# Kernel tuning notes

Hardware: AMD Instinct MI355X
Metric: run time of the kernel (lower is better)

Reference implementation:

```python
import jax, jax.numpy as jnp
import numpy as np

N = 50000
E = 800000
P = 800000
DIN = 128
HID = 32
HEADS = 4
DOUT = 128
NEG_SLOPE = 0.2


def _gat_conv(x, src, dst, W, a_src, a_dst, bias, heads, C, n):
    # x: [n, in], W: [in, heads*C], a_src/a_dst: [heads, C], bias: [heads*C]
    xw = (x @ W).reshape(n, heads, C)
    alpha_s = (xw * a_src).sum(-1)  # [n, heads]
    alpha_d = (xw * a_dst).sum(-1)  # [n, heads]
    logits = jax.nn.leaky_relu(alpha_s[src] + alpha_d[dst], NEG_SLOPE)  # [e, heads]
    amax = jax.ops.segment_max(logits, dst, num_segments=n)
    ex = jnp.exp(logits - amax[dst])
    denom = jax.ops.segment_sum(ex, dst, num_segments=n)
    alpha = ex / denom[dst]  # segment softmax over incoming edges
    out = jax.ops.segment_sum(xw[src] * alpha[:, :, None], dst, num_segments=n)
    return out.reshape(n, heads * C) + bias


def setup_inputs() -> dict:
    key = jax.random.key(0)
    ks = jax.random.split(key, 16)
    s = 0.05
    inp = {
        "x": jax.random.normal(ks[0], (N, DIN), dtype=jnp.float32),
        "edge_index": jax.random.randint(ks[1], (2, E), 0, N, dtype=jnp.int32),
        "edge_pairs": jax.random.randint(ks[2], (2, P), 0, N, dtype=jnp.int32),
        "W1": jax.random.normal(ks[3], (DIN, HEADS * HID), dtype=jnp.float32) * s,
        "a_src1": jax.random.normal(ks[4], (HEADS, HID), dtype=jnp.float32) * s,
        "a_dst1": jax.random.normal(ks[5], (HEADS, HID), dtype=jnp.float32) * s,
        "b1": jnp.zeros((HEADS * HID,), dtype=jnp.float32),
        "W2": jax.random.normal(ks[6], (HEADS * HID, DOUT), dtype=jnp.float32) * s,
        "a_src2": jax.random.normal(ks[7], (1, DOUT), dtype=jnp.float32) * s,
        "a_dst2": jax.random.normal(ks[8], (1, DOUT), dtype=jnp.float32) * s,
        "b2": jnp.zeros((DOUT,), dtype=jnp.float32),
        "mw1": jax.random.normal(ks[9], (2 * DOUT, DOUT), dtype=jnp.float32) * s,
        "mb1": jnp.zeros((DOUT,), dtype=jnp.float32),
        "mw2": jax.random.normal(ks[10], (DOUT, DOUT // 2), dtype=jnp.float32) * s,
        "mb2": jnp.zeros((DOUT // 2,), dtype=jnp.float32),
        "mw3": jax.random.normal(ks[11], (DOUT // 2, 1), dtype=jnp.float32) * s,
        "mb3": jnp.zeros((1,), dtype=jnp.float32),
    }
    return inp


def reference(x, edge_index, edge_pairs, W1, a_src1, a_dst1, b1, W2, a_src2, a_dst2, b2, mw1, mb1, mw2, mb2, mw3, mb3):
    n = x.shape[0]
    loop = jnp.arange(n, dtype=edge_index.dtype)
    src = jnp.concatenate([edge_index[0], loop])  # add self loops (PyG default)
    dst = jnp.concatenate([edge_index[1], loop])
    h = _gat_conv(x, src, dst, W1, a_src1, a_dst1, b1, HEADS, HID, n)
    h = jax.nn.elu(h)
    z = _gat_conv(h, src, dst, W2, a_src2, a_dst2, b2, 1, DOUT, n)  # node embeddings [n, DOUT]
    zi = z[edge_pairs[0]]
    zj = z[edge_pairs[1]]
    e = jnp.concatenate([zi, zj], axis=-1)
    e = jax.nn.relu(e @ mw1 + mb1)  # dropout off (eval mode)
    e = jax.nn.relu(e @ mw2 + mb2)
    return jax.nn.sigmoid(e @ mw3 + mb3)  # [P, 1]
```

## Files before the change

### kernel.cpp

```cpp
#include <hip/hip_runtime.h>
#include <cstdint>
#include <cstddef>


#define NEG_SLOPE 0.2f

typedef __bf16 bf16x8 __attribute__((ext_vector_type(8)));
typedef float  f32x4  __attribute__((ext_vector_type(4)));

static __device__ __forceinline__ float bflo(unsigned pv) {
  return __uint_as_float(pv << 16);
}
static __device__ __forceinline__ float bfhi(unsigned pv) {
  return __uint_as_float(pv & 0xffff0000u);
}

__global__ __launch_bounds__(256) void cvt_bf16_kernel(
    const float* __restrict__ x, __bf16* __restrict__ y, int total)
{
  const int i = (blockIdx.x * 256 + threadIdx.x) * 4;
  if (i + 3 < total) {
    const float4 v = *(const float4*)&x[i];
    union { __bf16 b[4]; uint2 u2; } pk;
    pk.b[0] = (__bf16)v.x; pk.b[1] = (__bf16)v.y;
    pk.b[2] = (__bf16)v.z; pk.b[3] = (__bf16)v.w;
    *(uint2*)&y[i] = pk.u2;
  }
}

__global__ __launch_bounds__(256) void convw_kernel(
    const float* __restrict__ W1, const float* __restrict__ W2,
    const float* __restrict__ mw1, const float* __restrict__ mw2,
    __bf16* __restrict__ W1t, __bf16* __restrict__ W2t,
    __bf16* __restrict__ mw1t, __bf16* __restrict__ w2t)
{
  const int i = blockIdx.x * 256 + threadIdx.x;
  if (i < 16384) {
    const int nn = i >> 7, k = i & 127;
    W1t[i] = (__bf16)W1[k * 128 + nn];
    W2t[i] = (__bf16)W2[k * 128 + nn];
  }
  if (i < 32768) {
    const int j = i >> 7, k = i & 127;
    mw1t[i] = (__bf16)((j < 128) ? mw1[k * 128 + j]
                                 : mw1[(128 + k) * 128 + (j - 128)]);
  }
  if (i < 8192) {
    const int nn = i >> 7, k = i & 127;
    w2t[i] = (__bf16)mw2[k * 64 + nn];
  }
}

template<int NOUT>
__global__ __launch_bounds__(256) void nodegemm_kernel(
    const __bf16* __restrict__ A, const __bf16* __restrict__ Wt,
    __bf16* __restrict__ C, int n)
{
  constexpr int NT = NOUT / 64;
  const int tid = threadIdx.x;
  const int wave = tid >> 6, lane = tid & 63;
  const int l16 = lane & 15;
  const int kl  = (lane >> 4) << 3;
  const int r4  = (lane >> 4) << 2;
  const int n0  = wave * (NOUT / 4);
  const int rowbase = blockIdx.x * 32;

  bf16x8 a[2][4];
  #pragma unroll
  for (int mt = 0; mt < 2; ++mt) {
    int row = rowbase + mt * 16 + l16;
    if (row >= n) row = n - 1;
    const size_t rb = (size_t)row * 128;
    #pragma unroll
    for (int ks = 0; ks < 4; ++ks)
      a[mt][ks] = *(const bf16x8*)&A[rb + ks * 32 + kl];
  }
  f32x4 acc[2][NT];
  #pragma unroll
  for (int mt = 0; mt < 2; ++mt)
    #pragma unroll
    for (int nt = 0; nt < NT; ++nt) acc[mt][nt] = (f32x4){0.f, 0.f, 0.f, 0.f};

  #pragma unroll
  for (int ks = 0; ks < 4; ++ks) {
    #pragma unroll
    for (int nt = 0; nt < NT; ++nt) {
      const bf16x8 b =
          *(const bf16x8*)&Wt[(size_t)(n0 + nt * 16 + l16) * 128 + ks * 32 + kl];
      #pragma unroll
      for (int mt = 0; mt < 2; ++mt)
        acc[mt][nt] = __builtin_amdgcn_mfma_f32_16x16x32_bf16(
            a[mt][ks], b, acc[mt][nt], 0, 0, 0);
    }
  }
  #pragma unroll
  for (int mt = 0; mt < 2; ++mt) {
    #pragma unroll
    for (int nt = 0; nt < NT; ++nt) {
      const int col = n0 + nt * 16 + l16;
      #pragma unroll
      for (int j = 0; j < 4; ++j) {
        const int row = rowbase + mt * 16 + r4 + j;
        if (row < n) C[(size_t)row * NOUT + col] = (__bf16)acc[mt][nt][j];
      }
    }
  }
}

template<int HEADS>
__global__ __launch_bounds__(256) void alpha_kernel(
    const __bf16* __restrict__ xw, const float* __restrict__ a_src,
    const float* __restrict__ a_dst, float* __restrict__ as_out,
    float* __restrict__ ad_out, int n)
{
  const int node = blockIdx.x * 4 + (threadIdx.x >> 6);
  const int lane = threadIdx.x & 63;
  if (node >= n) return;
  const unsigned short* xwu = (const unsigned short*)xw;
  const float x1 = __uint_as_float((unsigned)xwu[(size_t)node * 128 + lane] << 16);
  const float x2 = __uint_as_float((unsigned)xwu[(size_t)node * 128 + lane + 64] << 16);
  float s1 = x1 * a_src[lane],      d1 = x1 * a_dst[lane];
  float s2 = x2 * a_src[lane + 64], d2 = x2 * a_dst[lane + 64];
  if (HEADS == 4) {
    #pragma unroll
    for (int m = 1; m <= 16; m <<= 1) {
      s1 += __shfl_xor(s1, m); d1 += __shfl_xor(d1, m);
      s2 += __shfl_xor(s2, m); d2 += __shfl_xor(d2, m);
    }
    if (lane == 0) {
      as_out[node * 4 + 0] = s1; as_out[node * 4 + 2] = s2;
      ad_out[node * 4 + 0] = d1; ad_out[node * 4 + 2] = d2;
    } else if (lane == 32) {
      as_out[node * 4 + 1] = s1; as_out[node * 4 + 3] = s2;
      ad_out[node * 4 + 1] = d1; ad_out[node * 4 + 3] = d2;
    }
  } else {
    float s = s1 + s2, d = d1 + d2;
    #pragma unroll
    for (int m = 1; m <= 32; m <<= 1) {
      s += __shfl_xor(s, m); d += __shfl_xor(d, m);
    }
    if (lane == 0) { as_out[node] = s; ad_out[node] = d; }
  }
}

__global__ __launch_bounds__(256) void hist_kernel(
    const int* __restrict__ ei, int* __restrict__ deg, int E, int n)
{
  const int e = blockIdx.x * 256 + threadIdx.x;
  if (e >= E + n) return;
  const int d = (e < E) ? ei[E + e] : e - E;
  atomicAdd(&deg[d], 1);
}

__global__ __launch_bounds__(256) void scan1_kernel(
    const int* __restrict__ deg, int* __restrict__ part,
    int* __restrict__ bsum, int n)
{
  __shared__ int s[256];
  const int i = blockIdx.x * 256 + threadIdx.x;
  s[threadIdx.x] = (i < n) ? deg[i] : 0;
  __syncthreads();
  #pragma unroll
  for (int off = 1; off < 256; off <<= 1) {
    const int t = (threadIdx.x >= off) ? s[threadIdx.x - off] : 0;
    __syncthreads();
    s[threadIdx.x] += t;
    __syncthreads();
  }
  if (i < n) part[i] = s[threadIdx.x];
  if (threadIdx.x == 255) bsum[blockIdx.x] = s[255];
}

__global__ __launch_bounds__(256) void scan2_kernel(int* __restrict__ bsum, int nb)
{
  __shared__ int s[256];
  s[threadIdx.x] = (threadIdx.x < nb) ? bsum[threadIdx.x] : 0;
  __syncthreads();
  #pragma unroll
  for (int off = 1; off < 256; off <<= 1) {
    const int t = (threadIdx.x >= off) ? s[threadIdx.x - off] : 0;
    __syncthreads();
    s[threadIdx.x] += t;
    __syncthreads();
  }
  const int excl = (threadIdx.x == 0) ? 0 : s[threadIdx.x - 1];
  if (threadIdx.x < nb) bsum[threadIdx.x] = excl;
}

__global__ __launch_bounds__(256) void scan3_kernel(
    const int* __restrict__ part, const int* __restrict__ bsum,
    int* __restrict__ rowptr, int n)
{
  const int i = blockIdx.x * 256 + threadIdx.x;
  if (i < n) rowptr[i + 1] = part[i] + bsum[blockIdx.x];
  if (i == 0) rowptr[0] = 0;
}

__global__ __launch_bounds__(256) void fill_kernel(
    const int* __restrict__ ei, const int* __restrict__ rowptr,
    int* __restrict__ cur, int* __restrict__ csr_src, int E, int n)
{
  const int e = blockIdx.x * 256 + threadIdx.x;
  if (e >= E + n) return;
  int s, d;
  if (e < E) { s = ei[e]; d = ei[E + e]; }
  else       { s = e - E; d = s; }
  const int pos = rowptr[d] + atomicAdd(&cur[d], 1);
  csr_src[pos] = s;
}

template<int HEADS, bool DO_ELU>
__global__ __launch_bounds__(256) void gat_gather_kernel(
    const int* __restrict__ csr_src, const int* __restrict__ rowptr,
    const __bf16* __restrict__ xw,
    const float* __restrict__ as_, const float* __restrict__ ad_,
    const float* __restrict__ bias,
    __bf16* __restrict__ out, int n)
{
  const int d = blockIdx.x * 4 + (threadIdx.x >> 6);
  if (d >= n) return;
  const int lane = threadIdx.x & 63;
  const int c0 = lane * 2;
  constexpr int C = 128 / HEADS;
  const int head = c0 / C;
  const float ad_d = ad_[d * HEADS + head];
  const int r0 = rowptr[d], r1 = rowptr[d + 1];
  float accx = 0.f, accy = 0.f, den = 0.f;

  int i = r0;
  for (; i + 4 <= r1; i += 4) {
    int s[4];
    #pragma unroll
    for (int u = 0; u < 4; ++u) s[u] = csr_src[i + u];
    float lg[4]; unsigned pv[4];
    #pragma unroll
    for (int u = 0; u < 4; ++u) {
      lg[u] = as_[s[u] * HEADS + head];
      pv[u] = *(const unsigned*)&xw[(size_t)s[u] * 128 + c0];
    }
    #pragma unroll
    for (int u = 0; u < 4; ++u) {
      float l = lg[u] + ad_d;
      l = (l > 0.f) ? l : NEG_SLOPE * l;
      const float ex = __expf(l);
      accx += ex * bflo(pv[u]); accy += ex * bfhi(pv[u]); den += ex;
    }
  }
  for (; i < r1; ++i) {
    const int s = csr_src[i];
    float l = as_[s * HEADS + head] + ad_d;
    l = (l > 0.f) ? l : NEG_SLOPE * l;
    const float ex = __expf(l);
    const unsigned pv = *(const unsigned*)&xw[(size_t)s * 128 + c0];
    accx += ex * bflo(pv); accy += ex * bfhi(pv); den += ex;
  }

  const float inv = 1.f / den;
  float rx = accx * inv + bias[c0];
  float ry = accy * inv + bias[c0 + 1];
  if (DO_ELU) {
    rx = rx > 0.f ? rx : expm1f(rx);
    ry = ry > 0.f ? ry : expm1f(ry);
  }
  union { __bf16 b[2]; unsigned u; } pk;
  pk.b[0] = (__bf16)rx; pk.b[1] = (__bf16)ry;
  *(unsigned*)&out[(size_t)d * 128 + c0] = pk.u;
}

__global__ __launch_bounds__(256) void pair_kernel(
    const __bf16* __restrict__ uv, const int* __restrict__ pairs,
    const float* __restrict__ mb1,
    const __bf16* __restrict__ w2t, const float* __restrict__ mb2,
    const float* __restrict__ mw3, const float* __restrict__ mb3,
    float* __restrict__ out, int P)
{
  const int tid = threadIdx.x;
  const int wave = tid >> 6, lane = tid & 63;
  const int l16 = lane & 15;
  const int kl  = (lane >> 4) << 3;
  const int r4  = (lane >> 4) << 2;
  const int mbase = blockIdx.x * 128 + wave * 32;

  size_t ib[2], jb[2];
  #pragma unroll
  for (int t = 0; t < 2; ++t) {
    int p = mbase + t * 16 + l16;
    if (p >= P) p = P - 1;
    ib[t] = (size_t)pairs[p] * 256;
    jb[t] = (size_t)pairs[P + p] * 256 + 128;
  }

  bf16x8 a[2][4];
  #pragma unroll
  for (int t = 0; t < 2; ++t) {
    bf16x8 uu[4], vv[4];
    #pragma unroll
    for (int s = 0; s < 4; ++s) {
      uu[s] = *(const bf16x8*)&uv[ib[t] + s * 32 + kl];
      vv[s] = *(const bf16x8*)&uv[jb[t] + s * 32 + kl];
    }
    #pragma unroll
    for (int s = 0; s < 4; ++s) {
      float bb[8];
      *(float4*)&bb[0] = *(const float4*)&mb1[s * 32 + kl];
      *(float4*)&bb[4] = *(const float4*)&mb1[s * 32 + kl + 4];
      #pragma unroll
      for (int e = 0; e < 8; ++e)
        a[t][s][e] = (__bf16)fmaxf((float)uu[s][e] + (float)vv[s][e] + bb[e], 0.f);
    }
  }

  f32x4 acc[2][4] = {};
  #pragma unroll
  for (int ks = 0; ks < 4; ++ks) {
    #pragma unroll
    for (int ni = 0; ni < 4; ++ni) {
      const bf16x8 b = *(const bf16x8*)&w2t[(size_t)(ni * 16 + l16) * 128 + ks * 32 + kl];
      #pragma unroll
      for (int t = 0; t < 2; ++t)
        acc[t][ni] = __builtin_amdgcn_mfma_f32_16x16x32_bf16(
            a[t][ks], b, acc[t][ni], 0, 0, 0);
    }
  }

  #pragma unroll
  for (int t = 0; t < 2; ++t) {
    float sum[4] = {0.f, 0.f, 0.f, 0.f};
    #pragma unroll
    for (int ni = 0; ni < 4; ++ni) {
      const int col = ni * 16 + l16;
      const float b2 = mb2[col];
      const float w3 = mw3[col];
      #pragma unroll
      for (int j = 0; j < 4; ++j)
        sum[j] += fmaxf(acc[t][ni][j] + b2, 0.f) * w3;
    }
    #pragma unroll
    for (int m = 1; m <= 8; m <<= 1) {
      #pragma unroll
      for (int j = 0; j < 4; ++j) sum[j] += __shfl_xor(sum[j], m);
    }
    if (l16 == 0) {
      const int p0 = mbase + t * 16 + r4;
      const float b3 = mb3[0];
      float4 o;
      o.x = 1.f / (1.f + expf(-(sum[0] + b3)));
      o.y = 1.f / (1.f + expf(-(sum[1] + b3)));
      o.z = 1.f / (1.f + expf(-(sum[2] + b3)));
      o.w = 1.f / (1.f + expf(-(sum[3] + b3)));
      if (p0 + 3 < P) {
        *(float4*)&out[p0] = o;
      } else {
        if (p0     < P) out[p0]     = o.x;
        if (p0 + 1 < P) out[p0 + 1] = o.y;
        if (p0 + 2 < P) out[p0 + 2] = o.z;
        if (p0 + 3 < P) out[p0 + 3] = o.w;
      }
    }
  }
}

extern "C" void kernel_launch(void* const* d_in, const int* in_sizes, int n_in,
                              void* d_out, int out_size, void* d_ws, size_t ws_size,
                              hipStream_t stream)
{
  const float* x   = (const float*)d_in[0];
  const int*   ei  = (const int*)d_in[1];
  const int*   ep  = (const int*)d_in[2];
  const float* W1  = (const float*)d_in[3];
  const float* as1 = (const float*)d_in[4];
  const float* ad1 = (const float*)d_in[5];
  const float* b1  = (const float*)d_in[6];
  const float* W2  = (const float*)d_in[7];
  const float* as2 = (const float*)d_in[8];
  const float* ad2 = (const float*)d_in[9];
  const float* b2  = (const float*)d_in[10];
  const float* mw1 = (const float*)d_in[11];
  const float* mb1 = (const float*)d_in[12];
  const float* mw2 = (const float*)d_in[13];
  const float* mb2 = (const float*)d_in[14];
  const float* mw3 = (const float*)d_in[15];
  const float* mb3 = (const float*)d_in[16];

  const int N = in_sizes[0] / 128;
  const int E = in_sizes[1] / 2;
  const int P = in_sizes[2] / 2;
  const int EN = E + N;

  __bf16* x_bf  = (__bf16*)d_ws;
  __bf16* xw_bf = x_bf  + (size_t)N * 128;
  __bf16* h_bf  = xw_bf + (size_t)N * 128;
  __bf16* uv_bf = h_bf  + (size_t)N * 128;
  __bf16* W1t   = uv_bf + (size_t)N * 256;
  __bf16* W2t   = W1t + 16384;
  __bf16* mw1t  = W2t + 16384;
  __bf16* w2t   = mw1t + 32768;
  float*  as_   = (float*)(w2t + 8192);
  float*  ad_   = as_ + (size_t)N * 4;
  int* rowptr   = (int*)(ad_ + (size_t)N * 4);
  int* deg      = rowptr + (N + 1);
  int* cur      = deg + N;
  int* part     = cur + N;
  int* bsum     = part + N;
  int* csr_src  = bsum + 256;
  __bf16* z_bf  = x_bf;
  float* out    = (float*)d_out;

  const int gEN = (EN + 255) / 256;
  const int nb  = (N + 255) / 256;
  const int gNG = (N + 31) / 32;

  hipMemsetAsync(deg, 0, (size_t)2 * N * sizeof(int), stream);
  hist_kernel <<<gEN, 256, 0, stream>>>(ei, deg, E, N);
  scan1_kernel<<<nb, 256, 0, stream>>>(deg, part, bsum, N);
  scan2_kernel<<<1, 256, 0, stream>>>(bsum, nb);
  scan3_kernel<<<nb, 256, 0, stream>>>(part, bsum, rowptr, N);
  fill_kernel <<<gEN, 256, 0, stream>>>(ei, rowptr, cur, csr_src, E, N);
  convw_kernel<<<128, 256, 0, stream>>>(W1, W2, mw1, mw2, W1t, W2t, mw1t, w2t);
  cvt_bf16_kernel<<<(N * 128 / 4 + 255) / 256, 256, 0, stream>>>(x, x_bf, N * 128);

  nodegemm_kernel<128><<<gNG, 256, 0, stream>>>(x_bf, W1t, xw_bf, N);
  alpha_kernel<4><<<(N + 3) / 4, 256, 0, stream>>>(xw_bf, as1, ad1, as_, ad_, N);
  gat_gather_kernel<4, true><<<(N + 3) / 4, 256, 0, stream>>>(
      csr_src, rowptr, xw_bf, as_, ad_, b1, h_bf, N);

  nodegemm_kernel<128><<<gNG, 256, 0, stream>>>(h_bf, W2t, xw_bf, N);
  alpha_kernel<1><<<(N + 3) / 4, 256, 0, stream>>>(xw_bf, as2, ad2, as_, ad_, N);
  gat_gather_kernel<1, false><<<(N + 3) / 4, 256, 0, stream>>>(
      csr_src, rowptr, xw_bf, as_, ad_, b2, z_bf, N);

  nodegemm_kernel<256><<<gNG, 256, 0, stream>>>(z_bf, mw1t, uv_bf, N);

  pair_kernel<<<(P + 127) / 128, 256, 0, stream>>>(
      uv_bf, ep, mb1, w2t, mb2, mw3, mb3, out, P);
}
```

Before: 471.5 us.

## Fuse fp32→bf16 conversion and attention-score dots into node GEMM epilogue

Removes the separate x conversion kernel by loading fp32 x directly in the first node GEMM and converting in registers. Computes the per-node source/destination attention scores inside the GEMM epilogue with shuffles (atomics for the single-head layer), eliminating both alpha kernels and their re-read of xw. Folds the mb1 bias into the third GEMM output so the pair kernel skips that add, and widens the gather unroll to 8 with masked tails. The fp32 loads double the A-read bytes in the first GEMM, and the float atomics make the layer-2 score accumulation order nondeterministic.

```diff
diff --git a/kernel.cpp b/kernel.cpp
--- a/kernel.cpp
+++ b/kernel.cpp
@@ -13,19 +13,6 @@
 }
 static __device__ __forceinline__ float bfhi(unsigned pv) {
   return __uint_as_float(pv & 0xffff0000u);
-}
-
-__global__ __launch_bounds__(256) void cvt_bf16_kernel(
-    const float* __restrict__ x, __bf16* __restrict__ y, int total)
-{
-  const int i = (blockIdx.x * 256 + threadIdx.x) * 4;
-  if (i + 3 < total) {
-    const float4 v = *(const float4*)&x[i];
-    union { __bf16 b[4]; uint2 u2; } pk;
-    pk.b[0] = (__bf16)v.x; pk.b[1] = (__bf16)v.y;
-    pk.b[2] = (__bf16)v.z; pk.b[3] = (__bf16)v.w;
-    *(uint2*)&y[i] = pk.u2;
-  }
 }
 
 __global__ __launch_bounds__(256) void convw_kernel(
@@ -51,10 +38,13 @@
   }
 }
 
-template<int NOUT>
+template<int NOUT, int HEADS, bool AF32, bool FOLDB>
 __global__ __launch_bounds__(256) void nodegemm_kernel(
-    const __bf16* __restrict__ A, const __bf16* __restrict__ Wt,
-    __bf16* __restrict__ C, int n)
+    const __bf16* __restrict__ A, const float* __restrict__ A32,
+    const __bf16* __restrict__ Wt, __bf16* __restrict__ C,
+    const float* __restrict__ asrc, const float* __restrict__ adst,
+    float* __restrict__ as_out, float* __restrict__ ad_out,
+    const float* __restrict__ vbias, int n)
 {
   constexpr int NT = NOUT / 64;
   const int tid = threadIdx.x;
@@ -72,8 +62,20 @@
     if (row >= n) row = n - 1;
     const size_t rb = (size_t)row * 128;
     #pragma unroll
-    for (int ks = 0; ks < 4; ++ks)
-      a[mt][ks] = *(const bf16x8*)&A[rb + ks * 32 + kl];
+    for (int ks = 0; ks < 4; ++ks) {
+      if (AF32) {
+        const float4 f0 = *(const float4*)&A32[rb + ks * 32 + kl];
+        const float4 f1 = *(const float4*)&A32[rb + ks * 32 + kl + 4];
+        bf16x8 t;
+        t[0] = (__bf16)f0.x; t[1] = (__bf16)f0.y;
+        t[2] = (__bf16)f0.z; t[3] = (__bf16)f0.w;
+        t[4] = (__bf16)f1.x; t[5] = (__bf16)f1.y;
+        t[6] = (__bf16)f1.z; t[7] = (__bf16)f1.w;
+        a[mt][ks] = t;
+      } else {
+        a[mt][ks] = *(const bf16x8*)&A[rb + ks * 32 + kl];
+      }
+    }
   }
   f32x4 acc[2][NT];
   #pragma unroll
@@ -93,54 +95,55 @@
             a[mt][ks], b, acc[mt][nt], 0, 0, 0);
     }
   }
+
   #pragma unroll
   for (int mt = 0; mt < 2; ++mt) {
     #pragma unroll
     for (int nt = 0; nt < NT; ++nt) {
       const int col = n0 + nt * 16 + l16;
+      float vb = 0.f;
+      if (FOLDB) vb = (col >= 128) ? vbias[col - 128] : 0.f;
       #pragma unroll
       for (int j = 0; j < 4; ++j) {
         const int row = rowbase + mt * 16 + r4 + j;
-        if (row < n) C[(size_t)row * NOUT + col] = (__bf16)acc[mt][nt][j];
+        if (row < n) C[(size_t)row * NOUT + col] = (__bf16)(acc[mt][nt][j] + vb);
       }
     }
   }
-}
-
-template<int HEADS>
-__global__ __launch_bounds__(256) void alpha_kernel(
-    const __bf16* __restrict__ xw, const float* __restrict__ a_src,
-    const float* __restrict__ a_dst, float* __restrict__ as_out,
-    float* __restrict__ ad_out, int n)
-{
-  const int node = blockIdx.x * 4 + (threadIdx.x >> 6);
-  const int lane = threadIdx.x & 63;
-  if (node >= n) return;
-  const unsigned short* xwu = (const unsigned short*)xw;
-  const float x1 = __uint_as_float((unsigned)xwu[(size_t)node * 128 + lane] << 16);
-  const float x2 = __uint_as_float((unsigned)xwu[(size_t)node * 128 + lane + 64] << 16);
-  float s1 = x1 * a_src[lane],      d1 = x1 * a_dst[lane];
-  float s2 = x2 * a_src[lane + 64], d2 = x2 * a_dst[lane + 64];
-  if (HEADS == 4) {
-    #pragma unroll
-    for (int m = 1; m <= 16; m <<= 1) {
-      s1 += __shfl_xor(s1, m); d1 += __shfl_xor(d1, m);
-      s2 += __shfl_xor(s2, m); d2 += __shfl_xor(d2, m);
-    }
-    if (lane == 0) {
-      as_out[node * 4 + 0] = s1; as_out[node * 4 + 2] = s2;
-      ad_out[node * 4 + 0] = d1; ad_out[node * 4 + 2] = d2;
-    } else if (lane == 32) {
-      as_out[node * 4 + 1] = s1; as_out[node * 4 + 3] = s2;
-      ad_out[node * 4 + 1] = d1; ad_out[node * 4 + 3] = d2;
-    }
-  } else {
-    float s = s1 + s2, d = d1 + d2;
-    #pragma unroll
-    for (int m = 1; m <= 32; m <<= 1) {
-      s += __shfl_xor(s, m); d += __shfl_xor(d, m);
-    }
-    if (lane == 0) { as_out[node] = s; ad_out[node] = d; }
+
+  if (HEADS > 0) {
+    float a_s[NT], a_d[NT];
+    #pragma unroll
+    for (int nt = 0; nt < NT; ++nt) {
+      const int col = n0 + nt * 16 + l16;
+      a_s[nt] = asrc[col]; a_d[nt] = adst[col];
+    }
+    #pragma unroll
+    for (int mt = 0; mt < 2; ++mt) {
+      #pragma unroll
+      for (int j = 0; j < 4; ++j) {
+        float ps = 0.f, pd = 0.f;
+        #pragma unroll
+        for (int nt = 0; nt < NT; ++nt) {
+          ps += acc[mt][nt][j] * a_s[nt];
+          pd += acc[mt][nt][j] * a_d[nt];
+        }
+        #pragma unroll
+        for (int m = 1; m <= 8; m <<= 1) {
+          ps += __shfl_xor(ps, m); pd += __shfl_xor(pd, m);
+        }
+        const int row = rowbase + mt * 16 + r4 + j;
+        if (l16 == 0 && row < n) {
+          if (HEADS == 4) {
+            as_out[row * 4 + wave] = ps;
+            ad_out[row * 4 + wave] = pd;
+          } else {
+            atomicAdd(&as_out[row], ps);
+            atomicAdd(&ad_out[row], pd);
+          }
+        }
+      }
+    }
   }
 }
 
@@ -228,32 +231,24 @@
   const int r0 = rowptr[d], r1 = rowptr[d + 1];
   float accx = 0.f, accy = 0.f, den = 0.f;
 
-  int i = r0;
-  for (; i + 4 <= r1; i += 4) {
-    int s[4];
-    #pragma unroll
-    for (int u = 0; u < 4; ++u) s[u] = csr_src[i + u];
-    float lg[4]; unsigned pv[4];
-    #pragma unroll
-    for (int u = 0; u < 4; ++u) {
+  for (int i = r0; i < r1; i += 8) {
+    int s[8];
+    #pragma unroll
+    for (int u = 0; u < 8; ++u)
+      s[u] = csr_src[(i + u < r1) ? i + u : r1 - 1];
+    float lg[8]; unsigned pv[8];
+    #pragma unroll
+    for (int u = 0; u < 8; ++u) {
       lg[u] = as_[s[u] * HEADS + head];
       pv[u] = *(const unsigned*)&xw[(size_t)s[u] * 128 + c0];
     }
     #pragma unroll
-    for (int u = 0; u < 4; ++u) {
+    for (int u = 0; u < 8; ++u) {
       float l = lg[u] + ad_d;
       l = (l > 0.f) ? l : NEG_SLOPE * l;
-      const float ex = __expf(l);
+      const float ex = (i + u < r1) ? __expf(l) : 0.f;
       accx += ex * bflo(pv[u]); accy += ex * bfhi(pv[u]); den += ex;
     }
-  }
-  for (; i < r1; ++i) {
-    const int s = csr_src[i];
-    float l = as_[s * HEADS + head] + ad_d;
-    l = (l > 0.f) ? l : NEG_SLOPE * l;
-    const float ex = __expf(l);
-    const unsigned pv = *(const unsigned*)&xw[(size_t)s * 128 + c0];
-    accx += ex * bflo(pv); accy += ex * bfhi(pv); den += ex;
   }
 
   const float inv = 1.f / den;
@@ -270,7 +265,6 @@
 
 __global__ __launch_bounds__(256) void pair_kernel(
     const __bf16* __restrict__ uv, const int* __restrict__ pairs,
-    const float* __restrict__ mb1,
     const __bf16* __restrict__ w2t, const float* __restrict__ mb2,
     const float* __restrict__ mw3, const float* __restrict__ mb3,
     float* __restrict__ out, int P)
@@ -302,12 +296,9 @@
     }
     #pragma unroll
     for (int s = 0; s < 4; ++s) {
-      float bb[8];
-      *(float4*)&bb[0] = *(const float4*)&mb1[s * 32 + kl];
-      *(float4*)&bb[4] = *(const float4*)&mb1[s * 32 + kl + 4];
       #pragma unroll
       for (int e = 0; e < 8; ++e)
-        a[t][s][e] = (__bf16)fmaxf((float)uu[s][e] + (float)vv[s][e] + bb[e], 0.f);
+        a[t][s][e] = (__bf16)fmaxf((float)uu[s][e] + (float)vv[s][e], 0.f);
     }
   }
 
@@ -345,10 +336,10 @@
       const int p0 = mbase + t * 16 + r4;
       const float b3 = mb3[0];
       float4 o;
-      o.x = 1.f / (1.f + expf(-(sum[0] + b3)));
-      o.y = 1.f / (1.f + expf(-(sum[1] + b3)));
-      o.z = 1.f / (1.f + expf(-(sum[2] + b3)));
-      o.w = 1.f / (1.f + expf(-(sum[3] + b3)));
+      o.x = 1.f / (1.f + __expf(-(sum[0] + b3)));
+      o.y = 1.f / (1.f + __expf(-(sum[1] + b3)));
+      o.z = 1.f / (1.f + __expf(-(sum[2] + b3)));
+      o.w = 1.f / (1.f + __expf(-(sum[3] + b3)));
       if (p0 + 3 < P) {
         *(float4*)&out[p0] = o;
       } else {
@@ -388,8 +379,8 @@
   const int P = in_sizes[2] / 2;
   const int EN = E + N;
 
-  __bf16* x_bf  = (__bf16*)d_ws;
-  __bf16* xw_bf = x_bf  + (size_t)N * 128;
+  __bf16* z_bf  = (__bf16*)d_ws;
+  __bf16* xw_bf = z_bf  + (size_t)N * 128;
   __bf16* h_bf  = xw_bf + (size_t)N * 128;
   __bf16* uv_bf = h_bf  + (size_t)N * 128;
   __bf16* W1t   = uv_bf + (size_t)N * 256;
@@ -398,40 +389,41 @@
   __bf16* w2t   = mw1t + 32768;
   float*  as_   = (float*)(w2t + 8192);
   float*  ad_   = as_ + (size_t)N * 4;
-  int* rowptr   = (int*)(ad_ + (size_t)N * 4);
-  int* deg      = rowptr + (N + 1);
-  int* cur      = deg + N;
-  int* part     = cur + N;
+  int*    deg   = (int*)(ad_ + (size_t)N * 4);
+  int*    cur   = deg + N;
+  float*  as2v  = (float*)(cur + N);
+  float*  ad2v  = as2v + N;
+  int* part     = (int*)(ad2v + N);
   int* bsum     = part + N;
-  int* csr_src  = bsum + 256;
-  __bf16* z_bf  = x_bf;
+  int* rowptr   = bsum + 256;
+  int* csr_src  = rowptr + (N + 1);
   float* out    = (float*)d_out;
 
   const int gEN = (EN + 255) / 256;
   const int nb  = (N + 255) / 256;
   const int gNG = (N + 31) / 32;
 
-  hipMemsetAsync(deg, 0, (size_t)2 * N * sizeof(int), stream);
+  (void)hipMemsetAsync(deg, 0, (size_t)4 * N * sizeof(int), stream);
   hist_kernel <<<gEN, 256, 0, stream>>>(ei, deg, E, N);
   scan1_kernel<<<nb, 256, 0, stream>>>(deg, part, bsum, N);
   scan2_kernel<<<1, 256, 0, stream>>>(bsum, nb);
   scan3_kernel<<<nb, 256, 0, stream>>>(part, bsum, rowptr, N);
   fill_kernel <<<gEN, 256, 0, stream>>>(ei, rowptr, cur, csr_src, E, N);
   convw_kernel<<<128, 256, 0, stream>>>(W1, W2, mw1, mw2, W1t, W2t, mw1t, w2t);
-  cvt_bf16_kernel<<<(N * 128 / 4 + 255) / 256, 256, 0, stream>>>(x, x_bf, N * 128);
-
-  nodegemm_kernel<128><<<gNG, 256, 0, stream>>>(x_bf, W1t, xw_bf, N);
-  alpha_kernel<4><<<(N + 3) / 4, 256, 0, stream>>>(xw_bf, as1, ad1, as_, ad_, N);
+
+  nodegemm_kernel<128, 4, true, false><<<gNG, 256, 0, stream>>>(
+      nullptr, x, W1t, xw_bf, as1, ad1, as_, ad_, nullptr, N);
   gat_gather_kernel<4, true><<<(N + 3) / 4, 256, 0, stream>>>(
       csr_src, rowptr, xw_bf, as_, ad_, b1, h_bf, N);
 
-  nodegemm_kernel<128><<<gNG, 256, 0, stream>>>(h_bf, W2t, xw_bf, N);
-  alpha_kernel<1><<<(N + 3) / 4, 256, 0, stream>>>(xw_bf, as2, ad2, as_, ad_, N);
+  nodegemm_kernel<128, 1, false, false><<<gNG, 256, 0, stream>>>(
+      h_bf, nullptr, W2t, xw_bf, as2, ad2, as2v, ad2v, nullptr, N);
   gat_gather_kernel<1, false><<<(N + 3) / 4, 256, 0, stream>>>(
-      csr_src, rowptr, xw_bf, as_, ad_, b2, z_bf, N);
-
-  nodegemm_kernel<256><<<gNG, 256, 0, stream>>>(z_bf, mw1t, uv_bf, N);
+      csr_src, rowptr, xw_bf, as2v, ad2v, b2, z_bf, N);
+
+  nodegemm_kernel<256, 0, false, true><<<gNG, 256, 0, stream>>>(
+      z_bf, nullptr, mw1t, uv_bf, nullptr, nullptr, nullptr, nullptr, mb1, N);
 
   pair_kernel<<<(P + 127) / 128, 256, 0, stream>>>(
-      uv_bf, ep, mb1, w2t, mb2, mw3, mb3, out, P);
-}
+      uv_bf, ep, w2t, mb2, mw3, mb3, out, P);
+}
```

Measured after the change: 451.0 us. 1.05x faster.
